# Performance work log

Measured on AMD Instinct MI355X. Metric: run time of the kernel, lower is better.

## Reference

```python
import jax, jax.numpy as jnp
import numpy as np

NUM_ITEMS = 50000
B = 512      # batch of (user, item) pairs
L = 50       # padded per-user item-list length
K = 20       # top_k: length of each context channel
H = 32       # hidden_dim
D = 32       # output_dim


def setup_inputs() -> dict:
    key = jax.random.key(0)
    ks = jax.random.split(key, 8)
    ctx = jax.random.normal(ks[0], (NUM_ITEMS, 10, K), dtype=jnp.float32)
    item_idxs = jax.random.randint(ks[1], (B,), 0, NUM_ITEMS)
    user_items = jax.random.randint(ks[2], (B, L), 0, NUM_ITEMS)
    user_lens = jax.random.randint(ks[3], (B,), 1, L + 1)  # ragged lengths in [1, L]
    W1 = jax.random.normal(ks[4], (5, 1, H), dtype=jnp.float32) * 0.1
    b1 = jnp.zeros((5, H), dtype=jnp.float32)
    W2 = jax.random.normal(ks[5], (5, H, D), dtype=jnp.float32) * 0.1
    b2 = jnp.zeros((5, D), dtype=jnp.float32)
    Wout = jax.random.normal(ks[6], (D, 1), dtype=jnp.float32) * 0.1
    bout = jnp.zeros((1,), dtype=jnp.float32)
    return dict(ctx=ctx, W1=W1, b1=b1, W2=W2, b2=b2, Wout=Wout, bout=bout,
                item_idxs=item_idxs, user_items=user_items, user_lens=user_lens)


def _item_rep(feat, W1, b1, W2, b2):
    """feat: [..., 10, K] context channels -> [..., 5*K, D] item representation.
    Channels (2c, 2c+1) go through com_{c+1}: a shared 1->H->D MLP applied to each
    scalar (unsqueeze(1) in the original), outputs of the two channels multiplied."""
    prefix = feat.shape[:-2]
    x = feat.reshape(prefix + (5, 2, K))                     # [..., 5, 2, K]
    w1 = W1[:, 0, :].reshape((5, 1, 1, H))                   # input_dim == 1
    h = jax.nn.relu(x[..., None] * w1 + b1.reshape((5, 1, 1, H)))   # [..., 5, 2, K, H]
    o = jnp.einsum('...cpkh,chd->...cpkd', h, W2) + b2.reshape((5, 1, 1, D))
    rep = o[..., 0, :, :] * o[..., 1, :, :]                  # [..., 5, K, D]
    return rep.reshape(prefix + (5 * K, D))


def reference(ctx, W1, b1, W2, b2, Wout, bout, item_idxs, user_items, user_lens):
    # Target-item representations: gather contexts then tiny MLPs. [B, 5K, D]
    item_rep = _item_rep(ctx[item_idxs], W1, b1, W2, b2)
    # Per-user item reps (padded ragged) and masked mean over the item list.
    u_rep = _item_rep(ctx[user_items], W1, b1, W2, b2)       # [B, L, 5K, D]
    mask = (jnp.arange(L)[None, :] < user_lens[:, None]).astype(u_rep.dtype)  # [B, L]
    u_mean = jnp.einsum('blnd,bl->bnd', u_rep, mask) / user_lens[:, None, None].astype(u_rep.dtype)
    inter = u_mean * item_rep                                # [B, 5K, D]
    pred = jax.nn.sigmoid(inter @ Wout + bout)               # [B, 5K, 1]
    return pred.reshape(B * 5 * K, 1)
```

## Files before the change

kernel.cpp:

```cpp
#include <hip/hip_runtime.h>
#include <math.h>

#define NITEMS 50000
#define BATCH  512
#define LLEN   50
#define KTOP   20
#define HDIM   32
#define DDIM   32
#define NCH    5
#define NSEG   33
#define NSCAL  200
#define NCELL  100
#define THRP   33
#define NWAVE  8
#define CSLOT  13

typedef _Float16 h2 __attribute__((ext_vector_type(2)));

static __device__ __forceinline__ float dot2_acc(h2 a, h2 b, float c) {
#if __has_builtin(__builtin_amdgcn_fdot2)
    return __builtin_amdgcn_fdot2(a, b, c, false);
#else
    return fmaf((float)a.x, (float)b.x, fmaf((float)a.y, (float)b.y, c));
#endif
}

#define WS_THRS  0
#define WS_AB16  160
#define WS_ORDER 5440


__global__ __launch_bounds__(256) void cnn_setup(
        const float* __restrict__ W1, const float* __restrict__ b1,
        const float* __restrict__ W2, const float* __restrict__ b2,
        const int* __restrict__ user_lens,
        float* __restrict__ ws, int* __restrict__ order) {
    const int tid = threadIdx.x;

    if (blockIdx.x < NSEG) {
        __shared__ float sW1[NCH*HDIM], sB1[NCH*HDIM], sThr[NCH*HDIM];
        __shared__ int   sRank[NCH*HDIM];
        __shared__ float sW2[NCH*HDIM*DDIM];
        __shared__ float sB2[NCH*DDIM];

        for (int i = tid; i < NCH*HDIM; i += 256) { sW1[i] = W1[i]; sB1[i] = b1[i]; }
        for (int i = tid; i < NCH*HDIM*DDIM; i += 256) sW2[i] = W2[i];
        for (int i = tid; i < NCH*DDIM; i += 256) sB2[i] = b2[i];
        __syncthreads();

        for (int i = tid; i < NCH*HDIM; i += 256) {
            float w = sW1[i];
            sThr[i] = (w != 0.f) ? (-sB1[i] / w) : INFINITY;
        }
        __syncthreads();

        for (int i = tid; i < NCH*HDIM; i += 256) {
            int c = i / HDIM, h = i % HDIM;
            float thr = sThr[i];
            int rank = 0;
            for (int h2i = 0; h2i < HDIM; ++h2i) {
                float thr2 = sThr[c*HDIM + h2i];
                rank += (thr2 < thr || (thr2 == thr && h2i < h)) ? 1 : 0;
            }
            sRank[i] = rank;
            if (blockIdx.x == 0) ws[WS_THRS + c*HDIM + rank] = thr;
        }
        __syncthreads();

        const int s = blockIdx.x;
        if (tid < NCH*DDIM) {
            int c = tid / DDIM, d = tid % DDIM;
            float A = 0.f, Bv = 0.f;
#pragma unroll
            for (int h = 0; h < HDIM; ++h) {
                float w  = sW1[c*HDIM + h];
                float bb = sB1[c*HDIM + h];
                int   r  = sRank[c*HDIM + h];
                bool active = (w > 0.f) ? (r < s) : ((w < 0.f) ? (r >= s) : (bb > 0.f));
                if (active) {
                    float w2 = sW2[(c*HDIM + h)*DDIM + d];
                    A  = fmaf(w,  w2, A);
                    Bv = fmaf(bb, w2, Bv);
                }
            }
            Bv += sB2[c*DDIM + d];
            unsigned short* ab = (unsigned short*)(ws + WS_AB16);
            int d4 = d >> 2, dd = d & 3;
            int base = ((c*NSEG + s)*32 + d4*4)*2;
            _Float16 ah = (_Float16)A, bh = (_Float16)Bv;
            ab[base + 4*(dd>>1) + (dd&1)]     = __builtin_bit_cast(unsigned short, ah);
            ab[base + 4*(dd>>1) + 2 + (dd&1)] = __builtin_bit_cast(unsigned short, bh);
        }
    } else {
        __shared__ int k512[BATCH], v512[BATCH];
        for (int i = tid; i < BATCH; i += 256) { k512[i] = user_lens[i]; v512[i] = i; }
        __syncthreads();
        for (int k = 2; k <= BATCH; k <<= 1) {
            for (int j = k >> 1; j > 0; j >>= 1) {
                int i   = ((tid & ~(j - 1)) << 1) | (tid & (j - 1));
                int ixj = i | j;
                bool up = ((i & k) == 0);
                int ka = k512[i], kb = k512[ixj];
                if ((ka > kb) == up) {
                    k512[i] = kb; k512[ixj] = ka;
                    int va = v512[i]; v512[i] = v512[ixj]; v512[ixj] = va;
                }
                __syncthreads();
            }
        }
        for (int i = tid; i < BATCH; i += 256) order[i] = v512[i];
    }
}

__global__ __launch_bounds__(512, 4) void cnn_main(
        const float* __restrict__ ctx,  const float* __restrict__ ws,
        const float* __restrict__ Wout, const float* __restrict__ bout,
        const int* __restrict__ item_idxs, const int* __restrict__ user_items,
        const int* __restrict__ user_lens, const int* __restrict__ order,
        float* __restrict__ out) {
    __shared__ unsigned int sAB16[NCH*NSEG*32];
    __shared__ float  sThrS[NCH*THRP];
    __shared__ uint2  sxo[NWAVE][NCELL];
    __shared__ uint2  sWt[NCELL*8];
    __shared__ float  pRed[NWAVE][NCELL];

    const int tid  = threadIdx.x;
    const int w    = tid >> 6;
    const int lane = tid & 63;
    const int g    = lane >> 3;
    const int d4   = lane & 7;

    const uint4* ABg = reinterpret_cast<const uint4*>(ws + WS_AB16);
    uint4* sAB4 = reinterpret_cast<uint4*>(sAB16);
    for (int i = tid; i < NCH*NSEG*8; i += 512) sAB4[i] = ABg[i];
    for (int i = tid; i < NCH*THRP; i += 512) {
        int c = i / THRP, j = i - c*THRP;
        sThrS[i] = (j < HDIM) ? ws[WS_THRS + c*HDIM + j] : 0.f;
    }

    const int rank = (blockIdx.x < 256) ? blockIdx.x : (767 - blockIdx.x);
    const int b    = order[rank];
    const int len  = user_lens[b];
    const float inv_len = 1.f / (float)len;
    const float bo = bout[0];
    const h2 wv0 = {(_Float16)Wout[4*d4],     (_Float16)Wout[4*d4 + 1]};
    const h2 wv1 = {(_Float16)Wout[4*d4 + 2], (_Float16)Wout[4*d4 + 3]};

    int sc[4], sdst[4];
#pragma unroll
    for (int r = 0; r < 4; ++r) {
        int idx  = lane + 64*r;
        int c    = idx / 40, rr = idx - c*40;
        int cell = c*KTOP + (rr % KTOP);
        sc[r]   = c;
        sdst[r] = cell*8 + (rr / KTOP)*4;
    }

    const int nstripe = (len > w) ? ((len - w + NWAVE - 1) / NWAVE) : 0;

    unsigned int wtA[CSLOT], wtB[CSLOT];
    float acc[CSLOT];
#pragma unroll
    for (int i = 0; i < CSLOT; ++i) acc[i] = 0.f;

    char* sxoB = (char*)&sxo[w][0];

    __syncthreads();

    float xp[4] = {0.f, 0.f, 0.f, 0.f};
    if (nstripe > 0) {
        const float* row = ctx + (size_t)user_items[b*LLEN + w] * NSCAL;
#pragma unroll
        for (int r = 0; r < 4; ++r) {
            int idx = lane + 64*r;
            if (idx < NSCAL) xp[r] = row[idx];
        }
    }

    if (w == 0) {
        float xt[4] = {0.f, 0.f, 0.f, 0.f};
        const float* row = ctx + (size_t)item_idxs[b] * NSCAL;
#pragma unroll
        for (int r = 0; r < 4; ++r) {
            int idx = lane + 64*r;
            if (idx < NSCAL) xt[r] = row[idx];
        }
#pragma unroll
        for (int r = 0; r < 4; ++r) {
            int idx = lane + 64*r;
            if (idx < NSCAL) {
                float xv = xt[r];
                int base = sc[r]*THRP;
                int pos = 0;
                pos += (sThrS[base + pos + 15] < xv) ? 16 : 0;
                pos += (sThrS[base + pos + 7]  < xv) ? 8  : 0;
                pos += (sThrS[base + pos + 3]  < xv) ? 4  : 0;
                pos += (sThrS[base + pos + 1]  < xv) ? 2  : 0;
                pos += (sThrS[base + pos]      < xv) ? 1  : 0;
                unsigned int off = (unsigned int)((sc[r]*NSEG + pos) << 7);
                _Float16 xh = (_Float16)xv;
                unsigned int word = (unsigned int)__builtin_bit_cast(unsigned short, xh)
                                  | (off << 16);
                *(unsigned int*)(sxoB + sdst[r]) = word;
            }
        }
        __builtin_amdgcn_wave_barrier();
#pragma unroll
        for (int i = 0; i < CSLOT; ++i) {
            int cell = g + 8*i;
            if (cell < NCELL) {
                uint2 xo = sxo[0][cell];
                const uint4* p0 = (const uint4*)((const char*)sAB16 + (xo.x >> 16) + (d4 << 4));
                const uint4* p1 = (const uint4*)((const char*)sAB16 + (xo.y >> 16) + (d4 << 4));
                uint4 q0 = *p0, q1 = *p1;
                _Float16 x0h = __builtin_bit_cast(_Float16, (unsigned short)(xo.x & 0xffffu));
                _Float16 x1h = __builtin_bit_cast(_Float16, (unsigned short)(xo.y & 0xffffu));
                h2 x0 = {x0h, x0h}, x1 = {x1h, x1h};
                h2 repa = (x0 * __builtin_bit_cast(h2, q0.x) + __builtin_bit_cast(h2, q0.y))
                        * (x1 * __builtin_bit_cast(h2, q1.x) + __builtin_bit_cast(h2, q1.y));
                h2 repb = (x0 * __builtin_bit_cast(h2, q0.z) + __builtin_bit_cast(h2, q0.w))
                        * (x1 * __builtin_bit_cast(h2, q1.z) + __builtin_bit_cast(h2, q1.w));
                wtA[i] = __builtin_bit_cast(unsigned int, (h2)(repa * wv0));
                wtB[i] = __builtin_bit_cast(unsigned int, (h2)(repb * wv1));
                sWt[cell*8 + d4] = make_uint2(wtA[i], wtB[i]);
            }
        }
    }
    __syncthreads();

    if (w != 0) {
#pragma unroll
        for (int i = 0; i < CSLOT; ++i) {
            int cell = g + 8*i;
            if (cell < NCELL) {
                uint2 v = sWt[cell*8 + d4];
                wtA[i] = v.x; wtB[i] = v.y;
            }
        }
    }

    for (int j = 0; j < nstripe; ++j) {
        float xc[4];
#pragma unroll
        for (int r = 0; r < 4; ++r) xc[r] = xp[r];

        if (j + 1 < nstripe) {
            const float* row = ctx + (size_t)user_items[b*LLEN + w + NWAVE*(j+1)] * NSCAL;
#pragma unroll
            for (int r = 0; r < 4; ++r) {
                int idx = lane + 64*r;
                if (idx < NSCAL) xp[r] = row[idx];
            }
        }

#pragma unroll
        for (int r = 0; r < 4; ++r) {
            int idx = lane + 64*r;
            if (idx < NSCAL) {
                float xv = xc[r];
                int base = sc[r]*THRP;
                int pos = 0;
                pos += (sThrS[base + pos + 15] < xv) ? 16 : 0;
                pos += (sThrS[base + pos + 7]  < xv) ? 8  : 0;
                pos += (sThrS[base + pos + 3]  < xv) ? 4  : 0;
                pos += (sThrS[base + pos + 1]  < xv) ? 2  : 0;
                pos += (sThrS[base + pos]      < xv) ? 1  : 0;
                unsigned int off = (unsigned int)((sc[r]*NSEG + pos) << 7);
                _Float16 xh = (_Float16)xv;
                unsigned int word = (unsigned int)__builtin_bit_cast(unsigned short, xh)
                                  | (off << 16);
                *(unsigned int*)(sxoB + sdst[r]) = word;
            }
        }
        __builtin_amdgcn_wave_barrier();

#pragma unroll
        for (int i = 0; i < CSLOT; ++i) {
            int cell = g + 8*i;
            if (cell < NCELL) {
                uint2 xo = sxo[w][cell];
                const uint4* p0 = (const uint4*)((const char*)sAB16 + (xo.x >> 16) + (d4 << 4));
                const uint4* p1 = (const uint4*)((const char*)sAB16 + (xo.y >> 16) + (d4 << 4));
                uint4 q0 = *p0, q1 = *p1;
                _Float16 x0h = __builtin_bit_cast(_Float16, (unsigned short)(xo.x & 0xffffu));
                _Float16 x1h = __builtin_bit_cast(_Float16, (unsigned short)(xo.y & 0xffffu));
                h2 x0 = {x0h, x0h}, x1 = {x1h, x1h};
                h2 repa = (x0 * __builtin_bit_cast(h2, q0.x) + __builtin_bit_cast(h2, q0.y))
                        * (x1 * __builtin_bit_cast(h2, q1.x) + __builtin_bit_cast(h2, q1.y));
                h2 repb = (x0 * __builtin_bit_cast(h2, q0.z) + __builtin_bit_cast(h2, q0.w))
                        * (x1 * __builtin_bit_cast(h2, q1.z) + __builtin_bit_cast(h2, q1.w));
                acc[i] = dot2_acc(repa, __builtin_bit_cast(h2, wtA[i]),
                         dot2_acc(repb, __builtin_bit_cast(h2, wtB[i]), acc[i]));
            }
        }
        __builtin_amdgcn_wave_barrier();
    }

#pragma unroll
    for (int i = 0; i < CSLOT; ++i) {
        int cell = g + 8*i;
        float v = acc[i];
        v += __shfl_xor(v, 1, 64);
        v += __shfl_xor(v, 2, 64);
        v += __shfl_xor(v, 4, 64);
        if (d4 == 0 && cell < NCELL) pRed[w][cell] = v;
    }
    __syncthreads();
    if (tid < NCELL) {
        float p = 0.f;
#pragma unroll
        for (int q = 0; q < NWAVE; ++q) p += pRed[q][tid];
        out[b*NCELL + tid] = 1.f / (1.f + expf(-(p*inv_len + bo)));
    }
}

extern "C" void kernel_launch(void* const* d_in, const int* in_sizes, int n_in,
                              void* d_out, int out_size, void* d_ws, size_t ws_size,
                              hipStream_t stream) {
    const float* ctx   = (const float*)d_in[0];
    const float* W1    = (const float*)d_in[1];
    const float* b1    = (const float*)d_in[2];
    const float* W2    = (const float*)d_in[3];
    const float* b2    = (const float*)d_in[4];
    const float* Wout  = (const float*)d_in[5];
    const float* bout  = (const float*)d_in[6];
    const int* item_idxs  = (const int*)d_in[7];
    const int* user_items = (const int*)d_in[8];
    const int* user_lens  = (const int*)d_in[9];
    float* out = (float*)d_out;
    float* ws  = (float*)d_ws;
    int*   order = (int*)(ws + WS_ORDER);

    cnn_setup<<<NSEG + 1, 256, 0, stream>>>(W1, b1, W2, b2, user_lens, ws, order);
    cnn_main<<<BATCH, 512, 0, stream>>>(ctx, ws, Wout, bout,
                                        item_idxs, user_items, user_lens,
                                        order, out);
}
```

Measured before the change: 115.3 us.

## Double-buffer per-wave staging and replace bitonic sort with counting sort

The per-row encode stage (threshold binary search and fp16 packing into shared memory) is now double-buffered per wave. The next row is encoded and the row after it is prefetched while the current buffer is consumed, so global loads and encoding can overlap with the compute loop. Separately, the setup kernel's bitonic sort of user lengths is replaced by a histogram-based counting sort using shared atomics, which needs far fewer barriers. The cost is more shared memory per block for the second buffer, which may reduce occupancy, and a non-stable ordering among users of equal length.

```diff
diff --git a/kernel.cpp b/kernel.cpp
--- a/kernel.cpp
+++ b/kernel.cpp
@@ -92,23 +92,20 @@
             ab[base + 4*(dd>>1) + 2 + (dd&1)] = __builtin_bit_cast(unsigned short, bh);
         }
     } else {
-        __shared__ int k512[BATCH], v512[BATCH];
-        for (int i = tid; i < BATCH; i += 256) { k512[i] = user_lens[i]; v512[i] = i; }
-        __syncthreads();
-        for (int k = 2; k <= BATCH; k <<= 1) {
-            for (int j = k >> 1; j > 0; j >>= 1) {
-                int i   = ((tid & ~(j - 1)) << 1) | (tid & (j - 1));
-                int ixj = i | j;
-                bool up = ((i & k) == 0);
-                int ka = k512[i], kb = k512[ixj];
-                if ((ka > kb) == up) {
-                    k512[i] = kb; k512[ixj] = ka;
-                    int va = v512[i]; v512[i] = v512[ixj]; v512[ixj] = va;
-                }
-                __syncthreads();
-            }
-        }
-        for (int i = tid; i < BATCH; i += 256) order[i] = v512[i];
+        __shared__ int sHist[LLEN + 1];
+        for (int i = tid; i <= LLEN; i += 256) sHist[i] = 0;
+        __syncthreads();
+        for (int i = tid; i < BATCH; i += 256) atomicAdd(&sHist[user_lens[i]], 1);
+        __syncthreads();
+        if (tid == 0) {
+            int accum = 0;
+            for (int l = 1; l <= LLEN; ++l) { int c = sHist[l]; sHist[l] = accum; accum += c; }
+        }
+        __syncthreads();
+        for (int i = tid; i < BATCH; i += 256) {
+            int pos = atomicAdd(&sHist[user_lens[i]], 1);
+            order[pos] = i;
+        }
     }
 }
 
@@ -120,7 +117,7 @@
         float* __restrict__ out) {
     __shared__ unsigned int sAB16[NCH*NSEG*32];
     __shared__ float  sThrS[NCH*THRP];
-    __shared__ uint2  sxo[NWAVE][NCELL];
+    __shared__ uint2  sxo[NWAVE][2][NCELL];
     __shared__ uint2  sWt[NCELL*8];
     __shared__ float  pRed[NWAVE][NCELL];
 
@@ -163,7 +160,7 @@
 #pragma unroll
     for (int i = 0; i < CSLOT; ++i) acc[i] = 0.f;
 
-    char* sxoB = (char*)&sxo[w][0];
+    char* sxoB = (char*)&sxo[w][0][0];
 
     __syncthreads();
 
@@ -209,7 +206,7 @@
         for (int i = 0; i < CSLOT; ++i) {
             int cell = g + 8*i;
             if (cell < NCELL) {
-                uint2 xo = sxo[0][cell];
+                uint2 xo = sxo[0][0][cell];
                 const uint4* p0 = (const uint4*)((const char*)sAB16 + (xo.x >> 16) + (d4 << 4));
                 const uint4* p1 = (const uint4*)((const char*)sAB16 + (xo.y >> 16) + (d4 << 4));
                 uint4 q0 = *p0, q1 = *p1;
@@ -239,25 +236,12 @@
         }
     }
 
-    for (int j = 0; j < nstripe; ++j) {
-        float xc[4];
-#pragma unroll
-        for (int r = 0; r < 4; ++r) xc[r] = xp[r];
-
-        if (j + 1 < nstripe) {
-            const float* row = ctx + (size_t)user_items[b*LLEN + w + NWAVE*(j+1)] * NSCAL;
-#pragma unroll
-            for (int r = 0; r < 4; ++r) {
-                int idx = lane + 64*r;
-                if (idx < NSCAL) xp[r] = row[idx];
-            }
-        }
-
+    if (nstripe > 0) {
 #pragma unroll
         for (int r = 0; r < 4; ++r) {
             int idx = lane + 64*r;
             if (idx < NSCAL) {
-                float xv = xc[r];
+                float xv = xp[r];
                 int base = sc[r]*THRP;
                 int pos = 0;
                 pos += (sThrS[base + pos + 15] < xv) ? 16 : 0;
@@ -272,13 +256,25 @@
                 *(unsigned int*)(sxoB + sdst[r]) = word;
             }
         }
+        if (nstripe > 1) {
+            const float* row = ctx + (size_t)user_items[b*LLEN + w + NWAVE] * NSCAL;
+#pragma unroll
+            for (int r = 0; r < 4; ++r) {
+                int idx = lane + 64*r;
+                if (idx < NSCAL) xp[r] = row[idx];
+            }
+        }
+    }
+
+    for (int j = 0; j < nstripe; ++j) {
         __builtin_amdgcn_wave_barrier();
 
+        const uint2* bufC = &sxo[w][j & 1][0];
 #pragma unroll
         for (int i = 0; i < CSLOT; ++i) {
             int cell = g + 8*i;
             if (cell < NCELL) {
-                uint2 xo = sxo[w][cell];
+                uint2 xo = bufC[cell];
                 const uint4* p0 = (const uint4*)((const char*)sAB16 + (xo.x >> 16) + (d4 << 4));
                 const uint4* p1 = (const uint4*)((const char*)sAB16 + (xo.y >> 16) + (d4 << 4));
                 uint4 q0 = *p0, q1 = *p1;
@@ -291,6 +287,37 @@
                         * (x1 * __builtin_bit_cast(h2, q1.z) + __builtin_bit_cast(h2, q1.w));
                 acc[i] = dot2_acc(repa, __builtin_bit_cast(h2, wtA[i]),
                          dot2_acc(repb, __builtin_bit_cast(h2, wtB[i]), acc[i]));
+            }
+        }
+
+        if (j + 1 < nstripe) {
+            int bofs = ((j + 1) & 1) * (NCELL * 8);
+#pragma unroll
+            for (int r = 0; r < 4; ++r) {
+                int idx = lane + 64*r;
+                if (idx < NSCAL) {
+                    float xv = xp[r];
+                    int base = sc[r]*THRP;
+                    int pos = 0;
+                    pos += (sThrS[base + pos + 15] < xv) ? 16 : 0;
+                    pos += (sThrS[base + pos + 7]  < xv) ? 8  : 0;
+                    pos += (sThrS[base + pos + 3]  < xv) ? 4  : 0;
+                    pos += (sThrS[base + pos + 1]  < xv) ? 2  : 0;
+                    pos += (sThrS[base + pos]      < xv) ? 1  : 0;
+                    unsigned int off = (unsigned int)((sc[r]*NSEG + pos) << 7);
+                    _Float16 xh = (_Float16)xv;
+                    unsigned int word = (unsigned int)__builtin_bit_cast(unsigned short, xh)
+                                      | (off << 16);
+                    *(unsigned int*)(sxoB + bofs + sdst[r]) = word;
+                }
+            }
+            if (j + 2 < nstripe) {
+                const float* row = ctx + (size_t)user_items[b*LLEN + w + NWAVE*(j+2)] * NSCAL;
+#pragma unroll
+                for (int r = 0; r < 4; ++r) {
+                    int idx = lane + 64*r;
+                    if (idx < NSCAL) xp[r] = row[idx];
+                }
             }
         }
         __builtin_amdgcn_wave_barrier();
```

New measurement: 190.5 us. +65.2%, slower.
